# Optimization experiments

Measured on AMD Instinct MI355X. Metric: run time of the kernel, lower is better.

The kernel has to match this reference:

```python
import jax, jax.numpy as jnp
import numpy as np

B, NS, NF, T, D = 64, 2, 13, 24, 512
H = 8
DH = D // H
DFF = 2048
EPS = 1e-5


def setup_inputs() -> dict:
    key = jax.random.key(0)
    ks = jax.random.split(key, 16)
    s = 0.02
    inp = {
        'x': jax.random.normal(ks[0], (B, NS * NF, T, D), jnp.float32),
        'w_in_s': jax.random.normal(ks[1], (3 * D, D), jnp.float32) * s,
        'b_in_s': jnp.zeros((3 * D,), jnp.float32),
        'w_out_s': jax.random.normal(ks[2], (D, D), jnp.float32) * s,
        'b_out_s': jnp.zeros((D,), jnp.float32),
        'w_in_f': jax.random.normal(ks[3], (3 * D, D), jnp.float32) * s,
        'b_in_f': jnp.zeros((3 * D,), jnp.float32),
        'w_out_f': jax.random.normal(ks[4], (D, D), jnp.float32) * s,
        'b_out_f': jnp.zeros((D,), jnp.float32),
        'w1': jax.random.normal(ks[5], (DFF, D), jnp.float32) * s,
        'b1': jnp.zeros((DFF,), jnp.float32),
        'w2': jax.random.normal(ks[6], (D, DFF), jnp.float32) * s,
        'b2': jnp.zeros((D,), jnp.float32),
        'g1': jnp.ones((D,), jnp.float32), 'be1': jnp.zeros((D,), jnp.float32),
        'g2': jnp.ones((D,), jnp.float32), 'be2': jnp.zeros((D,), jnp.float32),
        'g3': jnp.ones((D,), jnp.float32), 'be3': jnp.zeros((D,), jnp.float32),
    }
    return inp


def _layer_norm(x, g, b):
    mu = jnp.mean(x, axis=-1, keepdims=True)
    var = jnp.mean(jnp.square(x - mu), axis=-1, keepdims=True)
    return (x - mu) * jax.lax.rsqrt(var + EPS) * g + b


def _mha(x, w_in, b_in, w_out, b_out):
    # x: [..., S, D]; torch nn.MultiheadAttention math, eval mode (no dropout)
    qkv = x @ w_in.T + b_in                     # [..., S, 3D]
    q, k, v = jnp.split(qkv, 3, axis=-1)
    shp = q.shape[:-1] + (H, DH)
    q, k, v = q.reshape(shp), k.reshape(shp), v.reshape(shp)
    scores = jnp.einsum('...qhd,...khd->...hqk', q, k) / np.sqrt(DH).astype(np.float32)
    a = jax.nn.softmax(scores, axis=-1)
    o = jnp.einsum('...hqk,...khd->...qhd', a, v).reshape(x.shape)
    return o @ w_out.T + b_out


def reference(x, w_in_s, b_in_s, w_out_s, b_out_s, w_in_f, b_in_f, w_out_f, b_out_f,
              w1, b1, w2, b2, g1, be1, g2, be2, g3, be3):
    xr = x.reshape(B, NS, NF, T, D)
    # station attention: attend over the NS axis for each (feature, t)
    xs = xr.transpose(0, 2, 3, 1, 4)            # [B, NF, T, NS, D]
    xs = xs + _mha(xs, w_in_s, b_in_s, w_out_s, b_out_s)
    x = xs.transpose(0, 3, 1, 2, 4).reshape(B, NS * NF, T, D)
    x = _layer_norm(x, g1, be1)
    # feature attention: attend over the NF axis for each (station, t)
    xr = x.reshape(B, NS, NF, T, D)
    xf = xr.transpose(0, 1, 3, 2, 4)            # [B, NS, T, NF, D]
    xf = xf + _mha(xf, w_in_f, b_in_f, w_out_f, b_out_f)
    x = xf.transpose(0, 1, 3, 2, 4).reshape(B, NS * NF, T, D)
    x = _layer_norm(x, g2, be2)
    # feed-forward
    ff = jax.nn.relu(x @ w1.T + b1) @ w2.T + b2
    x = _layer_norm(x + ff, g3, be3)
    return x
```

## Files before the change

### kernel.cpp

```cpp
#include <hip/hip_runtime.h>
#include <stdint.h>

typedef unsigned short u16;
typedef __bf16 bf16x8 __attribute__((ext_vector_type(8)));
typedef float f32x4 __attribute__((ext_vector_type(4)));

#define DEV __device__ __forceinline__

DEV float bf2f(u16 u) {
    union { uint32_t u; float f; } c; c.u = ((uint32_t)u) << 16; return c.f;
}
DEV u16 f2bf(float f) {
    union { float f; uint32_t u; } c; c.f = f;
    uint32_t u = c.u;
    u += 0x7FFFu + ((u >> 16) & 1u);
    return (u16)(u >> 16);
}

DEV void gload_lds16(const u16* gp, u16* lp) {
    __builtin_amdgcn_global_load_lds(
        (__attribute__((address_space(1))) u16*)(uintptr_t)gp,
        (__attribute__((address_space(3))) u16*)lp,
        16, 0, 0);
}

DEV void load16f(const u16* p, float* f) {
    uint4 a = *reinterpret_cast<const uint4*>(p);
    uint4 b = *reinterpret_cast<const uint4*>(p + 8);
    uint32_t w[8] = { a.x, a.y, a.z, a.w, b.x, b.y, b.z, b.w };
#pragma unroll
    for (int k = 0; k < 8; ++k) {
        union { uint32_t u; float f; } lo, hi;
        lo.u = w[k] << 16; hi.u = w[k] & 0xFFFF0000u;
        f[2 * k] = lo.f; f[2 * k + 1] = hi.f;
    }
}
DEV float dot16(const u16* p, const float* q) {
    uint4 a = *reinterpret_cast<const uint4*>(p);
    uint4 b = *reinterpret_cast<const uint4*>(p + 8);
    uint32_t w[8] = { a.x, a.y, a.z, a.w, b.x, b.y, b.z, b.w };
    float d = 0.0f;
#pragma unroll
    for (int k = 0; k < 8; ++k) {
        union { uint32_t u; float f; } lo, hi;
        lo.u = w[k] << 16; hi.u = w[k] & 0xFFFF0000u;
        d += q[2 * k] * lo.f;
        d += q[2 * k + 1] * hi.f;
    }
    return d;
}
DEV void fma16(const u16* p, float pw, float* acc) {
    uint4 a = *reinterpret_cast<const uint4*>(p);
    uint4 b = *reinterpret_cast<const uint4*>(p + 8);
    uint32_t w[8] = { a.x, a.y, a.z, a.w, b.x, b.y, b.z, b.w };
#pragma unroll
    for (int k = 0; k < 8; ++k) {
        union { uint32_t u; float f; } lo, hi;
        lo.u = w[k] << 16; hi.u = w[k] & 0xFFFF0000u;
        acc[2 * k] += pw * lo.f;
        acc[2 * k + 1] += pw * hi.f;
    }
}
DEV void store16(u16* p, const float* y) {
    uint32_t w[8];
#pragma unroll
    for (int k = 0; k < 8; ++k)
        w[k] = (uint32_t)f2bf(y[2 * k]) | ((uint32_t)f2bf(y[2 * k + 1]) << 16);
    uint4 a = { w[0], w[1], w[2], w[3] };
    uint4 b = { w[4], w[5], w[6], w[7] };
    *reinterpret_cast<uint4*>(p) = a;
    *reinterpret_cast<uint4*>(p + 8) = b;
}

__global__ __launch_bounds__(256) void k_f32_to_bf16(
    const float* __restrict__ in, u16* __restrict__ out, int n4)
{
    int i = blockIdx.x * 256 + threadIdx.x;
    if (i >= n4) return;
    float4 v = reinterpret_cast<const float4*>(in)[i];
    ushort4 o;
    o.x = f2bf(v.x); o.y = f2bf(v.y); o.z = f2bf(v.z); o.w = f2bf(v.w);
    reinterpret_cast<ushort4*>(out)[i] = o;
}

template<bool RELU, bool RESID>
__global__ __launch_bounds__(256) void k_gemm(
    const u16* __restrict__ A, const u16* __restrict__ W,
    const float* __restrict__ bias, const u16* __restrict__ res,
    u16* __restrict__ C, int M, int N, int K)
{
    __shared__ __align__(16) u16 As[128 * 32];
    __shared__ __align__(16) u16 Bs[128 * 32];

    const int tid  = threadIdx.x;
    const int lane = tid & 63;
    const int wave = tid >> 6;
    const int wm   = wave >> 1;
    const int wn   = wave & 1;
    const long tileM = (long)blockIdx.y * 128;
    const long tileN = (long)blockIdx.x * 128;

    f32x4 acc[4][4] = {};

    const int r4 = tid >> 2;
    const int c8 = (tid & 3) * 8;
    const u16* Ab = A + (tileM + r4) * (long)K + c8;
    const u16* Wb = W + (tileN + r4) * (long)K + c8;
    u16* ldsA0 = As + wave * 512;
    u16* ldsA1 = As + 2048 + wave * 512;
    u16* ldsB0 = Bs + wave * 512;
    u16* ldsB1 = Bs + 2048 + wave * 512;

    const int arow = wm * 64 + (lane & 15);
    const int brow = wn * 64 + (lane & 15);
    const int kc   = (lane >> 4) * 8;

    for (int kk = 0; kk < K; kk += 32) {
        gload_lds16(Ab + kk,                 ldsA0);
        gload_lds16(Ab + kk + (long)64 * K,  ldsA1);
        gload_lds16(Wb + kk,                 ldsB0);
        gload_lds16(Wb + kk + (long)64 * K,  ldsB1);
        __syncthreads();

        bf16x8 a[4], b[4];
#pragma unroll
        for (int f = 0; f < 4; ++f) {
            a[f] = *reinterpret_cast<const bf16x8*>(&As[(arow + f * 16) * 32 + kc]);
            b[f] = *reinterpret_cast<const bf16x8*>(&Bs[(brow + f * 16) * 32 + kc]);
        }
#pragma unroll
        for (int i = 0; i < 4; ++i)
#pragma unroll
            for (int j = 0; j < 4; ++j)
                acc[i][j] = __builtin_amdgcn_mfma_f32_16x16x32_bf16(
                    a[i], b[j], acc[i][j], 0, 0, 0);
        __syncthreads();
    }

    const int crow = (int)tileM + wm * 64 + ((lane >> 4) << 2);
    const int ccol = (int)tileN + wn * 64 + (lane & 15);
#pragma unroll
    for (int i = 0; i < 4; ++i) {
#pragma unroll
        for (int j = 0; j < 4; ++j) {
            const int col = ccol + j * 16;
            const float bv = bias[col];
#pragma unroll
            for (int r = 0; r < 4; ++r) {
                const long row = crow + i * 16 + r;
                float v = acc[i][j][r] + bv;
                if (RESID) v += bf2f(res[row * N + col]);
                if (RELU)  v = fmaxf(v, 0.0f);
                C[row * N + col] = f2bf(v);
            }
        }
    }
}

__global__ __launch_bounds__(256) void k_attn_s(
    const u16* __restrict__ qkv, u16* __restrict__ o)
{
    const int wave = threadIdx.x >> 6, lane = threadIdx.x & 63;
    const int g = blockIdx.x * 4 + wave;
    const int t = g % 24, bf = g / 24, f = bf % 13, b = bf / 13;
    const int base = b * 624 + f * 24 + t;
    const int h = lane >> 3, i = (lane >> 2) & 1, c = lane & 3;
    const int off = h * 64 + c * 16;

    float qf[16];
    load16f(qkv + (size_t)(base + i * 312) * 1536 + off, qf);

    float s[2];
#pragma unroll
    for (int j = 0; j < 2; ++j) {
        float d = dot16(qkv + (size_t)(base + j * 312) * 1536 + 512 + off, qf);
        d += __shfl_xor(d, 1);
        d += __shfl_xor(d, 2);
        s[j] = d * 0.125f;
    }
    const float m = fmaxf(s[0], s[1]);
    const float e0 = expf(s[0] - m), e1 = expf(s[1] - m);
    const float inv = 1.0f / (e0 + e1);
    const float p0 = e0 * inv, p1 = e1 * inv;

    float acc[16] = {};
    fma16(qkv + (size_t)base * 1536 + 1024 + off, p0, acc);
    fma16(qkv + (size_t)(base + 312) * 1536 + 1024 + off, p1, acc);

    store16(o + (size_t)(base + i * 312) * 512 + off, acc);
}

__global__ __launch_bounds__(256) void k_attn_f(
    const u16* __restrict__ qkv, u16* __restrict__ o)
{
    const int wave = threadIdx.x >> 6, lane = threadIdx.x & 63;
    const int p = blockIdx.x * 4 + wave;
    const int h = p & 7, g = p >> 3;
    const int t = g % 24, bs = g / 24, st = bs % 2, b = bs / 2;
    const int base = b * 624 + st * 312 + t;
    const int i = lane >> 2, c = lane & 3;
    const int iq = (i < 13) ? i : 12;
    const int off = h * 64 + c * 16;

    float qf[16];
    load16f(qkv + (size_t)(base + iq * 24) * 1536 + off, qf);

    float sc[13];
#pragma unroll
    for (int j = 0; j < 13; ++j) {
        float d = dot16(qkv + (size_t)(base + j * 24) * 1536 + 512 + off, qf);
        d += __shfl_xor(d, 1);
        d += __shfl_xor(d, 2);
        sc[j] = d * 0.125f;
    }
    float m = sc[0];
#pragma unroll
    for (int j = 1; j < 13; ++j) m = fmaxf(m, sc[j]);
    float den = 0.0f;
#pragma unroll
    for (int j = 0; j < 13; ++j) { sc[j] = expf(sc[j] - m); den += sc[j]; }
    const float inv = 1.0f / den;

    float acc[16] = {};
#pragma unroll
    for (int j = 0; j < 13; ++j)
        fma16(qkv + (size_t)(base + j * 24) * 1536 + 1024 + off, sc[j], acc);
#pragma unroll
    for (int e = 0; e < 16; ++e) acc[e] *= inv;

    if (i < 13)
        store16(o + (size_t)(base + i * 24) * 512 + off, acc);
}

template<bool OUTF32>
__global__ __launch_bounds__(256) void k_ln(
    const u16* __restrict__ in, const float* __restrict__ g,
    const float* __restrict__ be, u16* __restrict__ outb,
    float* __restrict__ outf)
{
    const int row  = blockIdx.x * 4 + (threadIdx.x >> 6);
    const int lane = threadIdx.x & 63;
    const u16* p = in + (size_t)row * 512 + lane * 8;

    uint4 va = *reinterpret_cast<const uint4*>(p);
    uint32_t ua[4] = { va.x, va.y, va.z, va.w };
    float x[8];
#pragma unroll
    for (int i = 0; i < 4; ++i) {
        x[2 * i]     = bf2f((u16)(ua[i] & 0xFFFFu));
        x[2 * i + 1] = bf2f((u16)(ua[i] >> 16));
    }
    float s = 0.f, sq = 0.f;
#pragma unroll
    for (int i = 0; i < 8; ++i) { s += x[i]; sq += x[i] * x[i]; }
#pragma unroll
    for (int off = 32; off; off >>= 1) {
        s  += __shfl_xor(s, off);
        sq += __shfl_xor(sq, off);
    }
    const float mean = s * (1.0f / 512.0f);
    const float var  = sq * (1.0f / 512.0f) - mean * mean;
    const float rstd = rsqrtf(var + 1e-5f);

    const int col = lane * 8;
    float4 g0 = *reinterpret_cast<const float4*>(g + col);
    float4 g1 = *reinterpret_cast<const float4*>(g + col + 4);
    float4 b0 = *reinterpret_cast<const float4*>(be + col);
    float4 b1 = *reinterpret_cast<const float4*>(be + col + 4);
    float gg[8] = { g0.x, g0.y, g0.z, g0.w, g1.x, g1.y, g1.z, g1.w };
    float bb[8] = { b0.x, b0.y, b0.z, b0.w, b1.x, b1.y, b1.z, b1.w };

    float y[8];
#pragma unroll
    for (int i = 0; i < 8; ++i) y[i] = (x[i] - mean) * rstd * gg[i] + bb[i];

    if (OUTF32) {
        float4 o0 = { y[0], y[1], y[2], y[3] };
        float4 o1 = { y[4], y[5], y[6], y[7] };
        reinterpret_cast<float4*>(outf + (size_t)row * 512 + col)[0] = o0;
        reinterpret_cast<float4*>(outf + (size_t)row * 512 + col + 4)[0] = o1;
    } else {
        uint32_t w[4];
#pragma unroll
        for (int i = 0; i < 4; ++i)
            w[i] = (uint32_t)f2bf(y[2 * i]) | ((uint32_t)f2bf(y[2 * i + 1]) << 16);
        uint4 ov = { w[0], w[1], w[2], w[3] };
        *reinterpret_cast<uint4*>(outb + (size_t)row * 512 + col) = ov;
    }
}

extern "C" void kernel_launch(void* const* d_in, const int* in_sizes, int n_in,
                              void* d_out, int out_size, void* d_ws, size_t ws_size,
                              hipStream_t stream)
{
    const float* x       = (const float*)d_in[0];
    const float* w_in_s  = (const float*)d_in[1];
    const float* b_in_s  = (const float*)d_in[2];
    const float* w_out_s = (const float*)d_in[3];
    const float* b_out_s = (const float*)d_in[4];
    const float* w_in_f  = (const float*)d_in[5];
    const float* b_in_f  = (const float*)d_in[6];
    const float* w_out_f = (const float*)d_in[7];
    const float* b_out_f = (const float*)d_in[8];
    const float* w1      = (const float*)d_in[9];
    const float* b1      = (const float*)d_in[10];
    const float* w2      = (const float*)d_in[11];
    const float* b2      = (const float*)d_in[12];
    const float* g1      = (const float*)d_in[13];
    const float* be1     = (const float*)d_in[14];
    const float* g2      = (const float*)d_in[15];
    const float* be2     = (const float*)d_in[16];
    const float* g3      = (const float*)d_in[17];
    const float* be3     = (const float*)d_in[18];

    const int R = 39936;
    u16* xb   = (u16*)d_ws;
    u16* buf1 = xb + (size_t)R * 512;
    u16* obuf = buf1 + (size_t)R * 1536;
    u16* wqs  = buf1 + (size_t)R * 2048;
    u16* wos  = wqs + 1536 * 512;
    u16* wqf  = wos + 512 * 512;
    u16* wof  = wqf + 1536 * 512;
    u16* w1b  = wof + 512 * 512;
    u16* w2b  = w1b + 2048 * 512;

    auto conv = [&](const float* src, u16* dst, int n) {
        int n4 = n / 4;
        k_f32_to_bf16<<<dim3((n4 + 255) / 256), dim3(256), 0, stream>>>(src, dst, n4);
    };
    conv(x,       xb,  R * 512);
    conv(w_in_s,  wqs, 1536 * 512);
    conv(w_out_s, wos, 512 * 512);
    conv(w_in_f,  wqf, 1536 * 512);
    conv(w_out_f, wof, 512 * 512);
    conv(w1,      w1b, 2048 * 512);
    conv(w2,      w2b, 512 * 2048);

    const dim3 blk(256);
    const int MT = R / 128;

    k_gemm<false, false><<<dim3(12, MT), blk, 0, stream>>>(
        xb, wqs, b_in_s, nullptr, buf1, R, 1536, 512);
    k_attn_s<<<dim3(19968 / 4), blk, 0, stream>>>(buf1, obuf);
    k_gemm<false, true><<<dim3(4, MT), blk, 0, stream>>>(
        obuf, wos, b_out_s, xb, xb, R, 512, 512);
    k_ln<false><<<dim3(R / 4), blk, 0, stream>>>(xb, g1, be1, xb, nullptr);

    k_gemm<false, false><<<dim3(12, MT), blk, 0, stream>>>(
        xb, wqf, b_in_f, nullptr, buf1, R, 1536, 512);
    k_attn_f<<<dim3(24576 / 4), blk, 0, stream>>>(buf1, obuf);
    k_gemm<false, true><<<dim3(4, MT), blk, 0, stream>>>(
        obuf, wof, b_out_f, xb, xb, R, 512, 512);
    k_ln<false><<<dim3(R / 4), blk, 0, stream>>>(xb, g2, be2, xb, nullptr);

    k_gemm<true, false><<<dim3(16, MT), blk, 0, stream>>>(
        xb, w1b, b1, nullptr, buf1, R, 2048, 512);
    k_gemm<false, true><<<dim3(4, MT), blk, 0, stream>>>(
        buf1, w2b, b2, xb, xb, R, 512, 2048);
    k_ln<true><<<dim3(R / 4), blk, 0, stream>>>(xb, g3, be3, nullptr, (float*)d_out);
}
```

Measured before the change: 737.0 us.

## Swizzle GEMM LDS layout and remap blocks to XCDs for L2 locality

The GEMM kernel now XOR-swizzles the k-chunk offset when writing and reading LDS tiles, to reduce bank conflicts on the 16-byte fragment loads. It also switches to a 1D grid and maps block ids so each of the 8 XCDs gets a contiguous band of 39 M-tiles, aiming to keep A rows reused in that XCD's L2. The mapping hardcodes R/128 = 312 = 8*39, so it only holds for this problem size.

```diff
diff --git a/kernel.cpp b/kernel.cpp
--- a/kernel.cpp
+++ b/kernel.cpp
@@ -83,7 +83,7 @@
     reinterpret_cast<ushort4*>(out)[i] = o;
 }
 
-template<bool RELU, bool RESID>
+template<bool RELU, bool RESID, int NT>
 __global__ __launch_bounds__(256) void k_gemm(
     const u16* __restrict__ A, const u16* __restrict__ W,
     const float* __restrict__ bias, const u16* __restrict__ res,
@@ -97,13 +97,17 @@
     const int wave = tid >> 6;
     const int wm   = wave >> 1;
     const int wn   = wave & 1;
-    const long tileM = (long)blockIdx.y * 128;
-    const long tileN = (long)blockIdx.x * 128;
+
+    const int bid = blockIdx.x;
+    const int xcd = bid & 7;
+    const int j0  = bid >> 3;
+    const long tileM = (long)(xcd * 39 + j0 / NT) * 128;
+    const long tileN = (long)(j0 % NT) * 128;
 
     f32x4 acc[4][4] = {};
 
     const int r4 = tid >> 2;
-    const int c8 = (tid & 3) * 8;
+    const int c8 = ((tid & 3) ^ ((tid >> 3) & 3)) * 8;
     const u16* Ab = A + (tileM + r4) * (long)K + c8;
     const u16* Wb = W + (tileN + r4) * (long)K + c8;
     u16* ldsA0 = As + wave * 512;
@@ -113,7 +117,7 @@
 
     const int arow = wm * 64 + (lane & 15);
     const int brow = wn * 64 + (lane & 15);
-    const int kc   = (lane >> 4) * 8;
+    const int koff = ((lane >> 4) ^ ((lane >> 1) & 3)) * 8;
 
     for (int kk = 0; kk < K; kk += 32) {
         gload_lds16(Ab + kk,                 ldsA0);
@@ -125,8 +129,8 @@
         bf16x8 a[4], b[4];
 #pragma unroll
         for (int f = 0; f < 4; ++f) {
-            a[f] = *reinterpret_cast<const bf16x8*>(&As[(arow + f * 16) * 32 + kc]);
-            b[f] = *reinterpret_cast<const bf16x8*>(&Bs[(brow + f * 16) * 32 + kc]);
+            a[f] = *reinterpret_cast<const bf16x8*>(&As[(arow + f * 16) * 32 + koff]);
+            b[f] = *reinterpret_cast<const bf16x8*>(&Bs[(brow + f * 16) * 32 + koff]);
         }
 #pragma unroll
         for (int i = 0; i < 4; ++i)
@@ -337,25 +341,24 @@
     conv(w2,      w2b, 512 * 2048);
 
     const dim3 blk(256);
-    const int MT = R / 128;
-
-    k_gemm<false, false><<<dim3(12, MT), blk, 0, stream>>>(
+
+    k_gemm<false, false, 12><<<dim3(312 * 12), blk, 0, stream>>>(
         xb, wqs, b_in_s, nullptr, buf1, R, 1536, 512);
     k_attn_s<<<dim3(19968 / 4), blk, 0, stream>>>(buf1, obuf);
-    k_gemm<false, true><<<dim3(4, MT), blk, 0, stream>>>(
+    k_gemm<false, true, 4><<<dim3(312 * 4), blk, 0, stream>>>(
         obuf, wos, b_out_s, xb, xb, R, 512, 512);
     k_ln<false><<<dim3(R / 4), blk, 0, stream>>>(xb, g1, be1, xb, nullptr);
 
-    k_gemm<false, false><<<dim3(12, MT), blk, 0, stream>>>(
+    k_gemm<false, false, 12><<<dim3(312 * 12), blk, 0, stream>>>(
         xb, wqf, b_in_f, nullptr, buf1, R, 1536, 512);
     k_attn_f<<<dim3(24576 / 4), blk, 0, stream>>>(buf1, obuf);
-    k_gemm<false, true><<<dim3(4, MT), blk, 0, stream>>>(
+    k_gemm<false, true, 4><<<dim3(312 * 4), blk, 0, stream>>>(
         obuf, wof, b_out_f, xb, xb, R, 512, 512);
     k_ln<false><<<dim3(R / 4), blk, 0, stream>>>(xb, g2, be2, xb, nullptr);
 
-    k_gemm<true, false><<<dim3(16, MT), blk, 0, stream>>>(
+    k_gemm<true, false, 16><<<dim3(312 * 16), blk, 0, stream>>>(
         xb, w1b, b1, nullptr, buf1, R, 2048, 512);
-    k_gemm<false, true><<<dim3(4, MT), blk, 0, stream>>>(
+    k_gemm<false, true, 4><<<dim3(312 * 4), blk, 0, stream>>>(
         buf1, w2b, b2, xb, xb, R, 512, 2048);
     k_ln<true><<<dim3(R / 4), blk, 0, stream>>>(xb, g3, be3, nullptr, (float*)d_out);
 }
```

After: 690.2 us. 6.4% less time.
